# Kernel optimization log

Hardware: AMD Instinct MI355X
Metric: run time of the kernel (lower is better)

## Reference

```python
import jax, jax.numpy as jnp
import numpy as np

B, L, D_MODEL = 8, 2048, 768
D_INNER, D_STATE, DT_RANK, K = 1536, 16, 48, 4


def setup_inputs() -> dict:
    key = jax.random.key(0)
    ks = jax.random.split(key, 9)
    s = 0.02
    return {
        "hidden_states": jax.random.normal(ks[0], (B, L, D_MODEL), jnp.float32),
        "W_in": jax.random.normal(ks[1], (D_MODEL, 2 * D_INNER), jnp.float32) * s,
        "conv_w": jax.random.normal(ks[2], (D_INNER, 1, K), jnp.float32) * s,
        "conv_b": jax.random.normal(ks[3], (D_INNER,), jnp.float32) * s,
        "W_x": jax.random.normal(ks[4], (DT_RANK + 2 * D_STATE, D_INNER), jnp.float32) * s,
        "W_dt": jax.random.normal(ks[5], (D_INNER, DT_RANK), jnp.float32) * s,
        "b_dt": jax.random.normal(ks[6], (D_INNER,), jnp.float32) * s,
        "A_log": jax.random.normal(ks[7], (D_INNER, D_STATE), jnp.float32),
        "D_param": jax.random.normal(ks[8], (D_INNER,), jnp.float32),
    }


def _mamba(hidden_states, W_in, conv_w, conv_b, W_x, W_dt, b_dt, A_log, D_param):
    # in_proj then chunk into ssm branch (x) and gating residual (res)
    xz = hidden_states @ W_in                      # (B, L, 2*d_inner)
    x, res = jnp.split(xz, 2, axis=-1)             # each (B, L, d_inner)

    # causal depthwise conv over time, then SiLU
    xc = x.transpose(0, 2, 1)                      # (B, C, L)
    xc = jax.lax.conv_general_dilated(
        xc, conv_w, window_strides=(1,), padding=[(K - 1, 0)],
        feature_group_count=D_INNER, dimension_numbers=("NCH", "OIH", "NCH"))
    x = jax.nn.silu(xc + conv_b[None, :, None]).transpose(0, 2, 1)  # (B, L, d_inner)

    # input-dependent SSM parameters
    x_dbl = x @ W_x.T                              # (B, L, dt_rank + 2*d_state)
    dt = jax.nn.softplus(x_dbl[..., :DT_RANK] @ W_dt.T + b_dt)      # (B, L, d_inner)
    Bm = x_dbl[..., DT_RANK:DT_RANK + D_STATE]     # (B, L, d_state)
    Cm = x_dbl[..., DT_RANK + D_STATE:]            # (B, L, d_state)
    A = -jnp.exp(A_log)                            # (d_inner, d_state)

    def step(h, inp):
        x_t, dt_t, B_t, C_t = inp                  # (B,d_inner),(B,d_inner),(B,d_state),(B,d_state)
        dA = jnp.exp(dt_t[..., None] * A)          # (B, d_inner, d_state)
        dBx = (dt_t * x_t)[..., None] * B_t[:, None, :]
        h = dA * h + dBx
        y = jnp.einsum("bds,bs->bd", h, C_t)
        return h, y

    xs = (x.transpose(1, 0, 2), dt.transpose(1, 0, 2),
          Bm.transpose(1, 0, 2), Cm.transpose(1, 0, 2))
    h0 = jnp.zeros((x.shape[0], D_INNER, D_STATE), x.dtype)
    _, ys = jax.lax.scan(step, h0, xs)             # ys: (L, B, d_inner)
    y = ys.transpose(1, 0, 2) + x * D_param        # skip term
    return y * jax.nn.silu(res)                    # gated output (B, L, d_inner)


def reference(hidden_states, W_in, conv_w, conv_b, W_x, W_dt, b_dt, A_log, D_param):
    return _mamba(hidden_states, W_in, conv_w, conv_b, W_x, W_dt, b_dt, A_log, D_param)
```

## Files before the change

### kernel.cpp

```cpp
#include <hip/hip_runtime.h>
#include <hip/hip_bf16.h>
#include <stdint.h>

#define B_SZ 8
#define L_SZ 2048
#define DM 768
#define DI 1536
#define DS 16
#define DR 48
#define M_SZ (B_SZ * L_SZ)
#define N1 (2 * DI)

#define NC 64
#define TC (L_SZ / NC)
#define CH (B_SZ * DI)
#define KS 6
#define NT2 (DM / 32)
#define L2E 1.44269504088896f

typedef short short8 __attribute__((ext_vector_type(8)));
typedef float f32x4 __attribute__((ext_vector_type(4)));
typedef float f32x2 __attribute__((ext_vector_type(2)));

__device__ __forceinline__ ushort f2b(float f) {
  __hip_bfloat16 h = __float2bfloat16(f);
  return *reinterpret_cast<ushort*>(&h);
}
__device__ __forceinline__ float b2f(ushort u) {
  __hip_bfloat16 h;
  *reinterpret_cast<ushort*>(&h) = u;
  return __bfloat162float(h);
}
__device__ __forceinline__ ushort f2h(float f) {
  _Float16 h = (_Float16)f;
  return *reinterpret_cast<ushort*>(&h);
}
__device__ __forceinline__ float h2f(ushort u) {
  _Float16 h;
  *reinterpret_cast<ushort*>(&h) = u;
  return (float)h;
}

__device__ __forceinline__ void gl16(const ushort* g, ushort* l) {
  __builtin_amdgcn_global_load_lds(
      (const __attribute__((address_space(1))) void*)g,
      (__attribute__((address_space(3))) void*)l, 16, 0, 0);
}


__global__ __launch_bounds__(256) void prep_all(const float4* __restrict__ hs4,
                                                const float* __restrict__ w_in,
                                                const float* __restrict__ wx_f,
                                                const float* __restrict__ wdt_f,
                                                ushort4* __restrict__ A1,
                                                ushort* __restrict__ wt,
                                                ushort* __restrict__ wx_b,
                                                ushort* __restrict__ wdt_p) {
  const int n4 = M_SZ * DM / 4;
  const int nT = 3072 * 96;
  const int nwx = 80 * DI;
  const int nwdt = DI * 64;
  int idx = blockIdx.x * 256 + threadIdx.x;
  if (idx < n4) {
    float4 v = hs4[idx];
    ushort4 o;
    o.x = f2b(v.x); o.y = f2b(v.y); o.z = f2b(v.z); o.w = f2b(v.w);
    A1[idx] = o;
  } else if (idx < n4 + nT) {
    int j = idx - n4;
    int n = j % 3072;
    int kb = (j / 3072) * 8;
    short8 o;
#pragma unroll
    for (int q = 0; q < 8; ++q) o[q] = (short)f2b(w_in[(size_t)(kb + q) * 3072 + n]);
    *(short8*)(wt + (size_t)n * DM + kb) = o;
  } else if (idx < n4 + nT + nwx) {
    int j = idx - n4 - nT;
    wx_b[j] = f2b(wx_f[j]);
  } else if (idx < n4 + nT + nwx + nwdt) {
    int j = idx - n4 - nT - nwx;
    int col = j >> 6, k = j & 63;
    wdt_p[j] = (k < DR) ? f2b(wdt_f[col * DR + k]) : (ushort)0;
  }
}


__global__ __launch_bounds__(512, 1) void gemm_xz(const ushort* __restrict__ A,
                                                  const ushort* __restrict__ Bt,
                                                  ushort* __restrict__ xout,
                                                  ushort* __restrict__ gateout) {
  __shared__ ushort lds[49152];

  const int t = threadIdx.x;
  const int lane = t & 63;
  const int wid = t >> 6;
  const int wm = wid >> 2, wn = wid & 3;
  const int r = lane & 15, hi = lane >> 4;

  const int g = blockIdx.x;
  const int xcd = g & 7;
  const int local = g >> 3;
  const int bx = xcd * 8 + local / 12;
  const int by = local % 12;
  const int bm = bx * 256;
  const int bn = by * 256;

  const ushort* gsrc[4];
  int ldso[4];
#pragma unroll
  for (int i = 0; i < 4; ++i) {
    int c = wid * 4 + i;
    if (c < 16)
      gsrc[i] = A + (size_t)(bm + c * 16 + r) * DM + hi * 8;
    else
      gsrc[i] = Bt + (size_t)(bn + (c - 16) * 16 + r) * DM + hi * 8;
    ldso[i] = c * 512;
  }

  f32x4 acc[8][4];
#pragma unroll
  for (int m = 0; m < 8; ++m)
#pragma unroll
    for (int n = 0; n < 4; ++n) acc[m][n] = f32x4{0.f, 0.f, 0.f, 0.f};

  ushort* b0 = lds;
  ushort* b1 = lds + 16384;
  ushort* b2 = lds + 32768;

#pragma unroll
  for (int i = 0; i < 4; ++i) gl16(gsrc[i], b0 + ldso[i]);
#pragma unroll
  for (int i = 0; i < 4; ++i) gl16(gsrc[i] + 32, b1 + ldso[i]);
  asm volatile("s_waitcnt vmcnt(4)" ::: "memory");
  __builtin_amdgcn_s_barrier();

  for (int kt = 0; kt < NT2; ++kt) {
    const bool stage = (kt + 2 < NT2);
    const int koff = (kt + 2) * 32;

    short8 bfr[4];
#pragma unroll
    for (int n = 0; n < 4; ++n)
      bfr[n] = *(const short8*)&b0[(16 + wn * 4 + n) * 512 + lane * 8];

#pragma unroll
    for (int q = 0; q < 2; ++q) {
      short8 afr[4];
#pragma unroll
      for (int m = 0; m < 4; ++m)
        afr[m] = *(const short8*)&b0[(wm * 8 + q * 4 + m) * 512 + lane * 8];

      if (stage) {
        gl16(gsrc[2 * q] + koff, b2 + ldso[2 * q]);
        gl16(gsrc[2 * q + 1] + koff, b2 + ldso[2 * q + 1]);
      }

      asm volatile("s_barrier" ::: "memory");

      __builtin_amdgcn_s_setprio(1);
#pragma unroll
      for (int m = 0; m < 4; ++m)
#pragma unroll
        for (int n = 0; n < 4; ++n)
          acc[q * 4 + m][n] =
              __builtin_amdgcn_mfma_f32_16x16x32_bf16(afr[m], bfr[n], acc[q * 4 + m][n], 0, 0, 0);
      __builtin_amdgcn_s_setprio(0);

      if (q == 1) {
        if (stage)
          asm volatile("s_waitcnt vmcnt(4)" ::: "memory");
        else
          asm volatile("s_waitcnt vmcnt(0)" ::: "memory");
      }
      asm volatile("s_barrier" ::: "memory");
    }

    ushort* tmp = b0; b0 = b1; b1 = b2; b2 = tmp;
  }

  const bool isx = (bn < DI);
  ushort* outp = isx ? xout : gateout;
  const int cbase = bn - (isx ? 0 : DI) + wn * 64;
#pragma unroll
  for (int mf = 0; mf < 8; ++mf)
#pragma unroll
    for (int nf = 0; nf < 4; ++nf) {
      int col = cbase + nf * 16 + r;
#pragma unroll
      for (int j = 0; j < 4; ++j) {
        int row = bm + wm * 128 + mf * 16 + hi * 4 + j;
        float v = acc[mf][nf][j];
        if (!isx) v = v / (1.f + __expf(-v));
        outp[(size_t)row * DI + col] = f2b(v);
      }
    }
}


__global__ __launch_bounds__(256) void conv_silu(const ushort* __restrict__ xp,
                                                 const float* __restrict__ cw,
                                                 const float* __restrict__ cb,
                                                 ushort* __restrict__ xc) {
  int tid = blockIdx.x * 256 + threadIdx.x;
  const int nd = DI / 8;
  int db = tid % nd;
  int row = tid / nd;
  int d0 = db * 8;
  int l = row & (L_SZ - 1);
  const ushort* base = xp + (size_t)row * DI + d0;
  short8 z8 = {0, 0, 0, 0, 0, 0, 0, 0};
  short8 x0 = *(const short8*)base;
  short8 xm1 = (l >= 1) ? *(const short8*)(base - DI) : z8;
  short8 xm2 = (l >= 2) ? *(const short8*)(base - 2 * DI) : z8;
  short8 xm3 = (l >= 3) ? *(const short8*)(base - 3 * DI) : z8;
  short8 o;
#pragma unroll
  for (int j = 0; j < 8; ++j) {
    float4 w = *(const float4*)(cw + (size_t)(d0 + j) * 4);
    float a = cb[d0 + j] + w.x * b2f((ushort)xm3[j]) + w.y * b2f((ushort)xm2[j]) +
              w.z * b2f((ushort)xm1[j]) + w.w * b2f((ushort)x0[j]);
    float s = a / (1.f + __expf(-a));
    o[j] = (short)f2b(s);
  }
  *(short8*)(xc + (size_t)row * DI + d0) = o;
}


__global__ __launch_bounds__(256) void xdbl_gemm(const ushort* __restrict__ xc,
                                                 const ushort* __restrict__ wx,
                                                 float* __restrict__ xdp) {
  int wave = blockIdx.x * 4 + (threadIdx.x >> 6);
  int ks = blockIdx.y;
  int lane = threadIdx.x & 63;
  int r = lane & 15, hi = lane >> 4;
  int row0 = wave * 16;
  f32x4 acc[5];
#pragma unroll
  for (int n = 0; n < 5; ++n) acc[n] = f32x4{0.f, 0.f, 0.f, 0.f};
  const int kbeg = ks * (DI / KS), kend = kbeg + DI / KS;
  for (int k0 = kbeg; k0 < kend; k0 += 32) {
    short8 a = *(const short8*)(xc + (size_t)(row0 + r) * DI + k0 + hi * 8);
#pragma unroll
    for (int n = 0; n < 5; ++n) {
      short8 b = *(const short8*)(wx + (size_t)(n * 16 + r) * DI + k0 + hi * 8);
      acc[n] = __builtin_amdgcn_mfma_f32_16x16x32_bf16(a, b, acc[n], 0, 0, 0);
    }
  }
  float* op = xdp + (size_t)ks * M_SZ * 80;
#pragma unroll
  for (int n = 0; n < 5; ++n)
#pragma unroll
    for (int j = 0; j < 4; ++j)
      op[(size_t)(row0 + hi * 4 + j) * 80 + n * 16 + r] = acc[n][j];
}

__global__ __launch_bounds__(256) void reduce_xd(const float4* __restrict__ xdp,
                                                 float4* __restrict__ xd) {
  int i = blockIdx.x * 256 + threadIdx.x;
  if (i >= M_SZ * 20) return;
  float4 s = xdp[i];
#pragma unroll
  for (int k = 1; k < KS; ++k) {
    float4 v = xdp[(size_t)k * M_SZ * 20 + i];
    s.x += v.x; s.y += v.y; s.z += v.z; s.w += v.w;
  }
  xd[i] = s;
}


__device__ __forceinline__ short8 pack8f(const float* p) {
  short8 v;
#pragma unroll
  for (int i = 0; i < 8; ++i) v[i] = (short)f2b(p[i]);
  return v;
}

__global__ __launch_bounds__(256) void dt_gemm(const float* __restrict__ xd,
                                               const ushort* __restrict__ wdtp,
                                               const float* __restrict__ bdt,
                                               ushort* __restrict__ dt) {
  int wave = blockIdx.x * 4 + (threadIdx.x >> 6);
  int lane = threadIdx.x & 63;
  int r = lane & 15, hi = lane >> 4;
  int row0 = wave * 16;
  int c0 = blockIdx.y * 64;

  float atmp[8];
  const float* ap = xd + (size_t)(row0 + r) * 80 + hi * 8;
  float4 q0 = *(const float4*)ap, q1 = *(const float4*)(ap + 4);
  atmp[0] = q0.x; atmp[1] = q0.y; atmp[2] = q0.z; atmp[3] = q0.w;
  atmp[4] = q1.x; atmp[5] = q1.y; atmp[6] = q1.z; atmp[7] = q1.w;
  short8 a0 = pack8f(atmp);
  short8 a1 = {0, 0, 0, 0, 0, 0, 0, 0};
  if (hi < 2) {
    const float* ap1 = xd + (size_t)(row0 + r) * 80 + 32 + hi * 8;
    float4 p0 = *(const float4*)ap1, p1 = *(const float4*)(ap1 + 4);
    atmp[0] = p0.x; atmp[1] = p0.y; atmp[2] = p0.z; atmp[3] = p0.w;
    atmp[4] = p1.x; atmp[5] = p1.y; atmp[6] = p1.z; atmp[7] = p1.w;
    a1 = pack8f(atmp);
  }

  f32x4 acc[4];
#pragma unroll
  for (int n = 0; n < 4; ++n) acc[n] = f32x4{0.f, 0.f, 0.f, 0.f};
#pragma unroll
  for (int n = 0; n < 4; ++n) {
    const ushort* wp = wdtp + (size_t)(c0 + n * 16 + r) * 64;
    short8 b0 = *(const short8*)(wp + hi * 8);
    short8 b1 = *(const short8*)(wp + 32 + hi * 8);
    acc[n] = __builtin_amdgcn_mfma_f32_16x16x32_bf16(a0, b0, acc[n], 0, 0, 0);
    acc[n] = __builtin_amdgcn_mfma_f32_16x16x32_bf16(a1, b1, acc[n], 0, 0, 0);
  }
#pragma unroll
  for (int n = 0; n < 4; ++n)
#pragma unroll
    for (int j = 0; j < 4; ++j) {
      int col = c0 + n * 16 + r;
      float z = acc[n][j] + bdt[col];
      float sp = (z > 20.f) ? z : __logf(1.f + __expf(z));
      dt[(size_t)(row0 + hi * 4 + j) * DI + col] = f2h(sp);
    }
}


__global__ __launch_bounds__(256) void scan_pass1(const ushort* __restrict__ dt,
                                                  const ushort* __restrict__ xc,
                                                  const float* __restrict__ xd,
                                                  const float* __restrict__ A_log,
                                                  float* __restrict__ hend,
                                                  float* __restrict__ sumdt) {
  const int d = blockIdx.x * 256 + threadIdx.x;
  const int c = blockIdx.y, b = blockIdx.z;
  const int t0 = c * TC;

  __shared__ float Bs[TC * 16];
  for (int i = threadIdx.x; i < TC * 16; i += 256) {
    int tt = i >> 4, s = i & 15;
    Bs[i] = xd[((size_t)(b * L_SZ + t0 + tt)) * 80 + DR + s];
  }

  f32x2 a2[8];
  const float4* al4 = (const float4*)(A_log + (size_t)d * DS);
#pragma unroll
  for (int q = 0; q < 4; ++q) {
    float4 v = al4[q];
    a2[2 * q] = f32x2{-__expf(v.x) * L2E, -__expf(v.y) * L2E};
    a2[2 * q + 1] = f32x2{-__expf(v.z) * L2E, -__expf(v.w) * L2E};
  }

  __syncthreads();

  f32x2 h2[8];
#pragma unroll
  for (int q = 0; q < 8; ++q) h2[q] = f32x2{0.f, 0.f};
  float sd = 0.f;

  const ushort* dtp = dt + ((size_t)b * L_SZ + t0) * DI + d;
  const ushort* xp = xc + ((size_t)b * L_SZ + t0) * DI + d;

  ushort dt0 = dtp[0], dt1 = dtp[DI];
  ushort xu0 = xp[0], xu1 = xp[DI];
  dtp += 2 * (size_t)DI; xp += 2 * (size_t)DI;
  const f32x4* bp4 = (const f32x4*)Bs;
#pragma unroll 2
  for (int tt = 0; tt < TC; ++tt) {
    ushort dtu = dt0, xu = xu0;
    dt0 = dt1; xu0 = xu1;
    dt1 = *dtp; xu1 = *xp;
    dtp += DI; xp += DI;
    float dtv = h2f(dtu);
    float xv = b2f(xu);
    sd += dtv;
    float dx = dtv * xv;
    f32x2 dts = f32x2{dtv, dtv};
    f32x2 dxs = f32x2{dx, dx};
#pragma unroll
    for (int q4 = 0; q4 < 4; ++q4) {
      f32x4 bq = bp4[q4];
#pragma unroll
      for (int hq = 0; hq < 2; ++hq) {
        int q = q4 * 2 + hq;
        f32x2 bv = f32x2{bq[2 * hq], bq[2 * hq + 1]};
        f32x2 arg, t2;
        asm("v_pk_mul_f32 %0, %1, %2" : "=v"(arg) : "v"(dts), "v"(a2[q]));
        float e0, e1;
        asm("v_exp_f32 %0, %1" : "=v"(e0) : "v"(arg[0]));
        asm("v_exp_f32 %0, %1" : "=v"(e1) : "v"(arg[1]));
        asm("v_pk_mul_f32 %0, %1, %2" : "=v"(t2) : "v"(dxs), "v"(bv));
        h2[q][0] = __builtin_fmaf(e0, h2[q][0], t2[0]);
        h2[q][1] = __builtin_fmaf(e1, h2[q][1], t2[1]);
      }
    }
    bp4 += 4;
  }

  const size_t ch = (size_t)b * DI + d;
  sumdt[ch * NC + c] = sd;
  f32x2* hp = (f32x2*)&hend[((size_t)c * CH + ch) * 16];
#pragma unroll
  for (int q = 0; q < 8; ++q) hp[q] = h2[q];
}


__global__ __launch_bounds__(256) void scan_pass2(const float* __restrict__ A_log,
                                                  const float* __restrict__ sumdt,
                                                  float* __restrict__ hbuf) {
  int idx = blockIdx.x * 256 + threadIdx.x;
  int ch = idx >> 4, s = idx & 15;
  int d = ch % DI;
  float A = -__expf(A_log[d * DS + s]);
  float h = 0.f;
  for (int c = 0; c < NC; ++c) {
    float* p = &hbuf[((size_t)c * CH + ch) * 16 + s];
    float he = *p;
    *p = h;
    float sd = sumdt[(size_t)ch * NC + c];
    h = __expf(A * sd) * h + he;
  }
}

__global__ __launch_bounds__(256) void scan_pass3(const ushort* __restrict__ dt,
                                                  const ushort* __restrict__ xc,
                                                  const float* __restrict__ xd,
                                                  const ushort* __restrict__ gateb,
                                                  const float* __restrict__ A_log,
                                                  const float* __restrict__ Dp,
                                                  const float* __restrict__ hstart,
                                                  float* __restrict__ out) {
  const int d = blockIdx.x * 256 + threadIdx.x;
  const int c = blockIdx.y, b = blockIdx.z;
  const int t0 = c * TC;

  __shared__ float Bs[TC * 16];
  __shared__ float Cs[TC * 16];
  for (int i = threadIdx.x; i < TC * 16; i += 256) {
    int tt = i >> 4, s = i & 15;
    size_t row = ((size_t)(b * L_SZ + t0 + tt)) * 80;
    Bs[i] = xd[row + DR + s];
    Cs[i] = xd[row + DR + DS + s];
  }

  f32x2 a2[8];
  const float4* al4 = (const float4*)(A_log + (size_t)d * DS);
#pragma unroll
  for (int q = 0; q < 4; ++q) {
    float4 v = al4[q];
    a2[2 * q] = f32x2{-__expf(v.x) * L2E, -__expf(v.y) * L2E};
    a2[2 * q + 1] = f32x2{-__expf(v.z) * L2E, -__expf(v.w) * L2E};
  }
  const float Dpv = Dp[d];

  const size_t ch = (size_t)b * DI + d;
  f32x2 h2[8];
  const f32x2* hp = (const f32x2*)&hstart[((size_t)c * CH + ch) * 16];
#pragma unroll
  for (int q = 0; q < 8; ++q) h2[q] = hp[q];

  __syncthreads();

  const ushort* dtp = dt + ((size_t)b * L_SZ + t0) * DI + d;
  const ushort* xp = xc + ((size_t)b * L_SZ + t0) * DI + d;
  const ushort* gp = gateb + ((size_t)b * L_SZ + t0) * DI + d;
  float* op = out + ((size_t)b * L_SZ + t0) * DI + d;

  ushort dt0 = dtp[0], dt1 = dtp[DI];
  ushort xu0 = xp[0], xu1 = xp[DI];
  ushort gu0 = gp[0], gu1 = gp[DI];
  dtp += 2 * (size_t)DI; xp += 2 * (size_t)DI; gp += 2 * (size_t)DI;
  const f32x4* bp4 = (const f32x4*)Bs;
  const f32x4* cp4 = (const f32x4*)Cs;
#pragma unroll 2
  for (int tt = 0; tt < TC; ++tt) {
    ushort dtu = dt0, xu = xu0, gu = gu0;
    dt0 = dt1; xu0 = xu1; gu0 = gu1;
    dt1 = *dtp; xu1 = *xp; gu1 = *gp;
    dtp += DI; xp += DI; gp += DI;
    float dtv = h2f(dtu);
    float xv = b2f(xu);
    float gv = b2f(gu);
    float dx = dtv * xv;
    f32x2 dts = f32x2{dtv, dtv};
    f32x2 dxs = f32x2{dx, dx};
    f32x2 ya = f32x2{0.f, 0.f}, yb = f32x2{0.f, 0.f};
#pragma unroll
    for (int q4 = 0; q4 < 4; ++q4) {
      f32x4 bq = bp4[q4];
      f32x4 cq = cp4[q4];
#pragma unroll
      for (int hq = 0; hq < 2; ++hq) {
        int q = q4 * 2 + hq;
        f32x2 bv = f32x2{bq[2 * hq], bq[2 * hq + 1]};
        f32x2 cv = f32x2{cq[2 * hq], cq[2 * hq + 1]};
        f32x2 arg, t2;
        asm("v_pk_mul_f32 %0, %1, %2" : "=v"(arg) : "v"(dts), "v"(a2[q]));
        float e0, e1;
        asm("v_exp_f32 %0, %1" : "=v"(e0) : "v"(arg[0]));
        asm("v_exp_f32 %0, %1" : "=v"(e1) : "v"(arg[1]));
        asm("v_pk_mul_f32 %0, %1, %2" : "=v"(t2) : "v"(dxs), "v"(bv));
        h2[q][0] = __builtin_fmaf(e0, h2[q][0], t2[0]);
        h2[q][1] = __builtin_fmaf(e1, h2[q][1], t2[1]);
        if (hq)
          asm("v_pk_fma_f32 %0, %1, %2, %0" : "+v"(yb) : "v"(h2[q]), "v"(cv));
        else
          asm("v_pk_fma_f32 %0, %1, %2, %0" : "+v"(ya) : "v"(h2[q]), "v"(cv));
      }
    }
    bp4 += 4; cp4 += 4;
    float y = (ya[0] + ya[1]) + (yb[0] + yb[1]);
    op[0] = (y + xv * Dpv) * gv;
    op += DI;
  }
}


extern "C" void kernel_launch(void* const* d_in, const int* in_sizes, int n_in,
                              void* d_out, int out_size, void* d_ws, size_t ws_size,
                              hipStream_t stream) {
  const float* hs     = (const float*)d_in[0];
  const float* W_in   = (const float*)d_in[1];
  const float* conv_w = (const float*)d_in[2];
  const float* conv_b = (const float*)d_in[3];
  const float* W_x    = (const float*)d_in[4];
  const float* W_dt   = (const float*)d_in[5];
  const float* b_dt   = (const float*)d_in[6];
  const float* A_log  = (const float*)d_in[7];
  const float* D_par  = (const float*)d_in[8];
  float* out = (float*)d_out;
  char* ws = (char*)d_ws;

  size_t o = 0;
  ushort* A1   = (ushort*)(ws + o); o += (size_t)M_SZ * DM * 2;
  ushort* Wt1  = (ushort*)(ws + o); o += (size_t)N1 * DM * 2;
  ushort* xpre = (ushort*)(ws + o); o += (size_t)M_SZ * DI * 2;
  ushort* gate = (ushort*)(ws + o); o += (size_t)M_SZ * DI * 2;
  ushort* xcv  = (ushort*)(ws + o); o += (size_t)M_SZ * DI * 2;
  float*  xdbl = (float*)(ws + o);  o += (size_t)M_SZ * 80 * 4;
  ushort* dtb  = (ushort*)(ws + o); o += (size_t)M_SZ * DI * 2;
  float*  xdp  = (float*)(ws + o);  o += (size_t)KS * M_SZ * 80 * 4;
  ushort* Wxb  = (ushort*)(ws + o); o += (size_t)80 * DI * 2;
  ushort* Wdtp = (ushort*)(ws + o); o += (size_t)DI * 64 * 2;
  if (ws_size < o) return;

  float* hbuf  = (float*)(ws + 0);
  float* sumdt = (float*)(ws + (size_t)NC * CH * 16 * 4);

  const int nprep = M_SZ * DM / 4 + 3072 * 96 + 80 * DI + DI * 64;
  prep_all<<<dim3((nprep + 255) / 256), dim3(256), 0, stream>>>(
      (const float4*)hs, W_in, W_x, W_dt, (ushort4*)A1, Wt1, Wxb, Wdtp);

  gemm_xz<<<dim3((M_SZ / 256) * (N1 / 256)), dim3(512), 0, stream>>>(A1, Wt1, xpre, gate);

  conv_silu<<<dim3(M_SZ * DI / 8 / 256), dim3(256), 0, stream>>>(xpre, conv_w, conv_b, xcv);

  xdbl_gemm<<<dim3(M_SZ / 64, KS), dim3(256), 0, stream>>>(xcv, Wxb, xdp);
  reduce_xd<<<dim3((M_SZ * 20 + 255) / 256), dim3(256), 0, stream>>>((const float4*)xdp, (float4*)xdbl);

  dt_gemm<<<dim3(M_SZ / 64, 24), dim3(256), 0, stream>>>(xdbl, Wdtp, b_dt, dtb);

  scan_pass1<<<dim3(DI / 256, NC, B_SZ), dim3(256), 0, stream>>>(dtb, xcv, xdbl, A_log, hbuf, sumdt);
  scan_pass2<<<dim3(CH * 16 / 256), dim3(256), 0, stream>>>(A_log, sumdt, hbuf);
  scan_pass3<<<dim3(DI / 256, NC, B_SZ), dim3(256), 0, stream>>>(dtb, xcv, xdbl, gate,
                                                                 A_log, D_par, hbuf, out);
}
```

Before: 412.1 us.

## Fuse causal conv+SiLU into x_dbl GEMM via swizzled LDS staging

Merges the depthwise causal conv + SiLU kernel into the x_dbl projection GEMM. Each block computes the conv output for its 64-row by 256-column tile, writes it to global memory for later scan passes, and also stores it into a swizzled shared-memory buffer that feeds the MFMA A operand directly. This drops one kernel launch and the global re-read of the conv output by the GEMM. In exchange it adds LDS use and a barrier, and each block's conv work is now serialized ahead of its matmul.

```diff
diff --git a/kernel.cpp b/kernel.cpp
--- a/kernel.cpp
+++ b/kernel.cpp
@@ -197,52 +197,78 @@
 }
 
 
-__global__ __launch_bounds__(256) void conv_silu(const ushort* __restrict__ xp,
+__global__ __launch_bounds__(256) void xdbl_conv(const ushort* __restrict__ xp,
                                                  const float* __restrict__ cw,
                                                  const float* __restrict__ cb,
-                                                 ushort* __restrict__ xc) {
-  int tid = blockIdx.x * 256 + threadIdx.x;
-  const int nd = DI / 8;
-  int db = tid % nd;
-  int row = tid / nd;
-  int d0 = db * 8;
-  int l = row & (L_SZ - 1);
-  const ushort* base = xp + (size_t)row * DI + d0;
-  short8 z8 = {0, 0, 0, 0, 0, 0, 0, 0};
-  short8 x0 = *(const short8*)base;
-  short8 xm1 = (l >= 1) ? *(const short8*)(base - DI) : z8;
-  short8 xm2 = (l >= 2) ? *(const short8*)(base - 2 * DI) : z8;
-  short8 xm3 = (l >= 3) ? *(const short8*)(base - 3 * DI) : z8;
-  short8 o;
-#pragma unroll
-  for (int j = 0; j < 8; ++j) {
-    float4 w = *(const float4*)(cw + (size_t)(d0 + j) * 4);
-    float a = cb[d0 + j] + w.x * b2f((ushort)xm3[j]) + w.y * b2f((ushort)xm2[j]) +
-              w.z * b2f((ushort)xm1[j]) + w.w * b2f((ushort)x0[j]);
-    float s = a / (1.f + __expf(-a));
-    o[j] = (short)f2b(s);
-  }
-  *(short8*)(xc + (size_t)row * DI + d0) = o;
-}
-
-
-__global__ __launch_bounds__(256) void xdbl_gemm(const ushort* __restrict__ xc,
                                                  const ushort* __restrict__ wx,
+                                                 ushort* __restrict__ xc,
                                                  float* __restrict__ xdp) {
-  int wave = blockIdx.x * 4 + (threadIdx.x >> 6);
-  int ks = blockIdx.y;
-  int lane = threadIdx.x & 63;
-  int r = lane & 15, hi = lane >> 4;
-  int row0 = wave * 16;
+  __shared__ ushort Af[32 * 544];
+
+  const int tid = threadIdx.x;
+  const int row0 = blockIdx.x * 64;
+  const int ks = blockIdx.y;
+  const int kbeg = ks * 256;
+
+  {
+    const int rg = tid >> 5;
+    const int c8 = tid & 31;
+    const int col_loc = c8 * 8;
+    const int col = kbeg + col_loc;
+    const int chunkc = col_loc >> 5;
+    const int hi_w = (col_loc & 31) >> 3;
+
+    float4 cwv[8];
+    float cbv[8];
+#pragma unroll
+    for (int e = 0; e < 8; ++e) {
+      cwv[e] = *(const float4*)(cw + (size_t)(col + e) * 4);
+      cbv[e] = cb[col + e];
+    }
+    short8 z8 = {0, 0, 0, 0, 0, 0, 0, 0};
+#pragma unroll
+    for (int j = 0; j < 8; ++j) {
+      int row = row0 + rg * 8 + j;
+      int l = row & (L_SZ - 1);
+      const ushort* base = xp + (size_t)row * DI + col;
+      short8 x0 = *(const short8*)base;
+      short8 xm1 = (l >= 1) ? *(const short8*)(base - DI) : z8;
+      short8 xm2 = (l >= 2) ? *(const short8*)(base - 2 * DI) : z8;
+      short8 xm3 = (l >= 3) ? *(const short8*)(base - 3 * DI) : z8;
+      short8 o;
+#pragma unroll
+      for (int e = 0; e < 8; ++e) {
+        float4 w = cwv[e];
+        float a = cbv[e] + w.x * b2f((ushort)xm3[e]) + w.y * b2f((ushort)xm2[e]) +
+                  w.z * b2f((ushort)xm1[e]) + w.w * b2f((ushort)x0[e]);
+        o[e] = (short)f2b(a / (1.f + __expf(-a)));
+      }
+      *(short8*)(xc + (size_t)row * DI + col) = o;
+      int row_loc = rg * 8 + j;
+      int chunk = (row_loc >> 4) * 8 + chunkc;
+      int lane_t = (hi_w << 4) | (row_loc & 15);
+      int slot = lane_t ^ (chunk & 7);
+      *(short8*)&Af[chunk * 544 + slot * 8] = o;
+    }
+  }
+  __syncthreads();
+
+  const int lane = tid & 63, wid = tid >> 6;
+  const int r = lane & 15, hi = lane >> 4;
+  const int row0w = row0 + wid * 16;
+
   f32x4 acc[5];
 #pragma unroll
   for (int n = 0; n < 5; ++n) acc[n] = f32x4{0.f, 0.f, 0.f, 0.f};
-  const int kbeg = ks * (DI / KS), kend = kbeg + DI / KS;
-  for (int k0 = kbeg; k0 < kend; k0 += 32) {
-    short8 a = *(const short8*)(xc + (size_t)(row0 + r) * DI + k0 + hi * 8);
+
+#pragma unroll
+  for (int k0 = 0; k0 < 8; ++k0) {
+    int chunk = wid * 8 + k0;
+    short8 a = *(const short8*)&Af[chunk * 544 + ((lane ^ (chunk & 7)) * 8)];
+    const int kk = kbeg + k0 * 32;
 #pragma unroll
     for (int n = 0; n < 5; ++n) {
-      short8 b = *(const short8*)(wx + (size_t)(n * 16 + r) * DI + k0 + hi * 8);
+      short8 b = *(const short8*)(wx + (size_t)(n * 16 + r) * DI + kk + hi * 8);
       acc[n] = __builtin_amdgcn_mfma_f32_16x16x32_bf16(a, b, acc[n], 0, 0, 0);
     }
   }
@@ -251,7 +277,7 @@
   for (int n = 0; n < 5; ++n)
 #pragma unroll
     for (int j = 0; j < 4; ++j)
-      op[(size_t)(row0 + hi * 4 + j) * 80 + n * 16 + r] = acc[n][j];
+      op[(size_t)(row0w + hi * 4 + j) * 80 + n * 16 + r] = acc[n][j];
 }
 
 __global__ __launch_bounds__(256) void reduce_xd(const float4* __restrict__ xdp,
@@ -550,9 +576,8 @@
 
   gemm_xz<<<dim3((M_SZ / 256) * (N1 / 256)), dim3(512), 0, stream>>>(A1, Wt1, xpre, gate);
 
-  conv_silu<<<dim3(M_SZ * DI / 8 / 256), dim3(256), 0, stream>>>(xpre, conv_w, conv_b, xcv);
-
-  xdbl_gemm<<<dim3(M_SZ / 64, KS), dim3(256), 0, stream>>>(xcv, Wxb, xdp);
+  xdbl_conv<<<dim3(M_SZ / 64, KS), dim3(256), 0, stream>>>(xpre, conv_w, conv_b, Wxb,
+                                                           xcv, xdp);
   reduce_xd<<<dim3((M_SZ * 20 + 255) / 256), dim3(256), 0, stream>>>((const float4*)xdp, (float4*)xdbl);
 
   dt_gemm<<<dim3(M_SZ / 64, 24), dim3(256), 0, stream>>>(xdbl, Wdtp, b_dt, dtb);
```

Result: faster. 364.7 us (-11.5%).
